# Kernel optimization log

Measured on AMD Instinct MI355X. Metric: run time of the kernel, lower is better.

## Reference

```python
import jax, jax.numpy as jnp
import numpy as np

N, C, E, H = 100000, 128, 640000, 128


def setup_inputs() -> dict:
    key = jax.random.key(0)
    ks = jax.random.split(key, 8)
    x = jax.random.normal(ks[0], (N, C), dtype=jnp.float32)
    # edges guaranteed to have no self-loops (module removes them then re-adds clean self-loops)
    rol = jax.random.randint(ks[1], (E,), 0, N, dtype=jnp.int32)
    off = jax.random.randint(ks[2], (E,), 1, N, dtype=jnp.int32)
    col = (rol + off) % N
    edge_index = jnp.stack([rol, col])  # [2, E]
    s = 1.0 / np.sqrt(C)
    return {
        "x": x,
        "edge_index": edge_index,
        "W_emb": jax.random.normal(ks[3], (C, C), dtype=jnp.float32) * s,
        "b_emb": jnp.zeros((C,), dtype=jnp.float32),
        "Wa1": jax.random.normal(ks[4], (C, H), dtype=jnp.float32) * s,
        "ba1": jnp.zeros((H,), dtype=jnp.float32),
        "Wa2": jax.random.normal(ks[5], (H, 1), dtype=jnp.float32) * (1.0 / np.sqrt(H)),
        "ba2": jnp.zeros((1,), dtype=jnp.float32),
        "W_upd": jax.random.normal(ks[6], (C, C), dtype=jnp.float32) * s,
        "b_upd": jnp.zeros((C,), dtype=jnp.float32),
    }


def reference(x, edge_index, W_emb, b_emb, Wa1, ba1, Wa2, ba2, W_upd, b_upd):
    n = x.shape[0]
    loops = jnp.arange(n, dtype=edge_index.dtype)
    rol = jnp.concatenate([edge_index[0], loops])  # [E+N]
    col = jnp.concatenate([edge_index[1], loops])

    embedded_x = x @ W_emb + b_emb                     # [N, C]
    diff = x[rol] - x[col]                             # [E+N, C]
    h = jax.nn.leaky_relu(diff @ Wa1 + ba1, 0.01)      # [E+N, H]
    a = h @ Wa2 + ba2                                  # [E+N, 1]

    # segment softmax over incoming edges of each target node (col)
    amax = jax.ops.segment_max(a, col, num_segments=n)     # [N, 1]
    ea = jnp.exp(a - amax[col])
    denom = jax.ops.segment_sum(ea, col, num_segments=n)   # [N, 1]
    w = ea / (denom[col] + 1e-16)                           # [E+N, 1]

    msg = jax.ops.segment_sum(embedded_x[rol] * w, col, num_segments=n)  # [N, C]
    return msg @ W_upd + b_upd
```

## Files before the change

### kernel.cpp

```cpp
#include <hip/hip_runtime.h>
#include <hip/hip_bf16.h>

#define LRELU(t) ((t) > 0.0f ? (t) : 0.01f * (t))

__device__ __forceinline__ unsigned short f2bf(float f) {
  unsigned u = __float_as_uint(f);
  u += 0x7fff + ((u >> 16) & 1);
  return (unsigned short)(u >> 16);
}
__device__ __forceinline__ float bflo(unsigned u) { return __uint_as_float(u << 16); }
__device__ __forceinline__ float bfhi(unsigned u) { return __uint_as_float(u & 0xffff0000u); }

template <bool BF16OUT>
__global__ __launch_bounds__(256) void gemm128_kernel(
    const float* __restrict__ A, int lda, const float* __restrict__ B,
    const float* __restrict__ bias, void* __restrict__ Cout, int ldo, int M) {
  __shared__ float Ws[64 * 128];
  __shared__ float Xs[64 * 64];
  const int t = threadIdx.x;
  const int row0 = blockIdx.x * 64;
  const int c0 = (t & 31) * 4;
  const int r0 = (t >> 5) * 8;
  float acc[8][4];
#pragma unroll
  for (int i = 0; i < 8; ++i)
#pragma unroll
    for (int j = 0; j < 4; ++j) acc[i][j] = 0.f;

  for (int kc = 0; kc < 2; ++kc) {
    const int k0 = kc * 64;
#pragma unroll
    for (int i = 0; i < 8; ++i) {
      int f = t + i * 256;
      float4 w4 = *reinterpret_cast<const float4*>(B + (size_t)k0 * 128 + f * 4);
      *reinterpret_cast<float4*>(&Ws[f * 4]) = w4;
    }
#pragma unroll
    for (int i = 0; i < 4; ++i) {
      int f = t + i * 256;
      int r = f >> 4, kq = f & 15;
      float4 x4 = make_float4(0.f, 0.f, 0.f, 0.f);
      int row = row0 + r;
      if (row < M) x4 = *reinterpret_cast<const float4*>(A + (size_t)row * lda + k0 + kq * 4);
      *reinterpret_cast<float4*>(&Xs[r * 64 + kq * 4]) = x4;
    }
    __syncthreads();
#pragma unroll 8
    for (int kk = 0; kk < 64; ++kk) {
      float4 b4 = *reinterpret_cast<const float4*>(&Ws[kk * 128 + c0]);
#pragma unroll
      for (int i = 0; i < 8; ++i) {
        float av = Xs[(r0 + i) * 64 + kk];
        acc[i][0] += av * b4.x;
        acc[i][1] += av * b4.y;
        acc[i][2] += av * b4.z;
        acc[i][3] += av * b4.w;
      }
    }
    __syncthreads();
  }
  float4 bs = make_float4(0.f, 0.f, 0.f, 0.f);
  if (bias) bs = *reinterpret_cast<const float4*>(bias + c0);
#pragma unroll
  for (int i = 0; i < 8; ++i) {
    int row = row0 + r0 + i;
    if (row < M) {
      float vx = acc[i][0] + bs.x, vy = acc[i][1] + bs.y;
      float vz = acc[i][2] + bs.z, vw = acc[i][3] + bs.w;
      if (BF16OUT) {
        ushort4 o;
        o.x = f2bf(vx); o.y = f2bf(vy); o.z = f2bf(vz); o.w = f2bf(vw);
        *reinterpret_cast<ushort4*>((unsigned short*)Cout + (size_t)row * ldo + c0) = o;
      } else {
        float4 o = make_float4(vx, vy, vz, vw);
        *reinterpret_cast<float4*>((float*)Cout + (size_t)row * ldo + c0) = o;
      }
    }
  }
}

__global__ void zero_kernel(int* __restrict__ p, int n) {
  int i = blockIdx.x * blockDim.x + threadIdx.x;
  if (i < n) p[i] = 0;
}

__global__ void count_kernel(const int* __restrict__ col, int* __restrict__ counts, int E) {
  int e = blockIdx.x * blockDim.x + threadIdx.x;
  if (e < E) atomicAdd(&counts[col[e]], 1);
}

__global__ __launch_bounds__(1024) void scan1_kernel(const int* __restrict__ counts,
                                                     int* __restrict__ offsets,
                                                     int* __restrict__ bsum, int N, int N1) {
  __shared__ int sh[1024];
  int tid = threadIdx.x;
  int i = blockIdx.x * 1024 + tid;
  int v = (i < N) ? counts[i] : 0;
  sh[tid] = v;
  __syncthreads();
  for (int off = 1; off < 1024; off <<= 1) {
    int tv = (tid >= off) ? sh[tid - off] : 0;
    __syncthreads();
    sh[tid] += tv;
    __syncthreads();
  }
  if (i < N1) offsets[i] = sh[tid] - v;
  if (tid == 1023) bsum[blockIdx.x] = sh[1023];
}

__global__ __launch_bounds__(128) void scan2_kernel(int* __restrict__ bsum, int NB) {
  __shared__ int sh[128];
  int tid = threadIdx.x;
  int v = (tid < NB) ? bsum[tid] : 0;
  sh[tid] = v;
  __syncthreads();
  for (int off = 1; off < 128; off <<= 1) {
    int tv = (tid >= off) ? sh[tid - off] : 0;
    __syncthreads();
    sh[tid] += tv;
    __syncthreads();
  }
  if (tid < NB) bsum[tid] = sh[tid] - v;
}

__global__ __launch_bounds__(1024) void scan3_kernel(int* __restrict__ offsets,
                                                     const int* __restrict__ bsum,
                                                     int* __restrict__ cursor, int N, int N1) {
  int i = blockIdx.x * 1024 + threadIdx.x;
  if (i < N1) {
    int o = offsets[i] + bsum[blockIdx.x];
    offsets[i] = o;
    if (i < N) cursor[i] = o;
  }
}

__global__ __launch_bounds__(64) void prep_kernel(const float* __restrict__ ba1,
                                                  const float* __restrict__ Wa2,
                                                  const float* __restrict__ ba2,
                                                  float* __restrict__ a_self) {
  int l = threadIdx.x;
  float t1 = ba1[l], t2 = ba1[l + 64];
  float v = LRELU(t1) * Wa2[l] + LRELU(t2) * Wa2[l + 64];
#pragma unroll
  for (int off = 32; off > 0; off >>= 1) v += __shfl_xor(v, off);
  if (l == 0) *a_self = v + ba2[0];
}

__global__ void scatter_kernel(const int* __restrict__ rol, const int* __restrict__ col,
                               int* __restrict__ cursor, int* __restrict__ csr_rol, int E) {
  int e = blockIdx.x * blockDim.x + threadIdx.x;
  if (e < E) {
    int pos = atomicAdd(&cursor[col[e]], 1);
    csr_rol[pos] = rol[e];
  }
}

__global__ __launch_bounds__(256) void fused_kernel(
    const int* __restrict__ offsets, const int* __restrict__ csr_rol,
    const unsigned* __restrict__ embP, const float2* __restrict__ ba1_2,
    const float2* __restrict__ Wa2_2, const float* __restrict__ ba2,
    const float* __restrict__ a_self_p, float* __restrict__ msg, int N, int nwt) {
  const int lane = threadIdx.x & 63;
  const int wid = blockIdx.x * (blockDim.x >> 6) + (threadIdx.x >> 6);
  const float2 b2 = ba1_2[lane];
  const float2 w2 = Wa2_2[lane];
  const float ba2v = *ba2;
  const float aself = *a_self_p;

#define LOGIT(pp) (LRELU(bflo(pp) - pcx + b2.x) * w2.x + LRELU(bfhi(pp) - pcy + b2.y) * w2.y)
#define ONLINE(aval, ue)                      \
  {                                           \
    float nm = fmaxf(m, (aval));              \
    float cc = __expf(m - nm);                \
    float w = __expf((aval)-nm);              \
    s = s * cc + w;                           \
    ax = ax * cc + w * bflo(ue);              \
    ay = ay * cc + w * bfhi(ue);              \
    m = nm;                                   \
  }

  for (int n = wid; n < N; n += nwt) {
    int j0 = offsets[n], j1 = offsets[n + 1];
    unsigned ue_own = embP[(size_t)n * 128 + lane];
    unsigned up_own = embP[(size_t)n * 128 + 64 + lane];
    float pcx = bflo(up_own), pcy = bfhi(up_own);
    float m = aself, s = 1.0f;
    float ax = bflo(ue_own), ay = bfhi(ue_own);
    int j = j0;
    for (; j + 4 <= j1; j += 4) {
      int r0 = csr_rol[j], r1 = csr_rol[j + 1], r2 = csr_rol[j + 2], r3 = csr_rol[j + 3];
      unsigned pe0 = embP[(size_t)r0 * 128 + lane];
      unsigned pp0 = embP[(size_t)r0 * 128 + 64 + lane];
      unsigned pe1 = embP[(size_t)r1 * 128 + lane];
      unsigned pp1 = embP[(size_t)r1 * 128 + 64 + lane];
      unsigned pe2 = embP[(size_t)r2 * 128 + lane];
      unsigned pp2 = embP[(size_t)r2 * 128 + 64 + lane];
      unsigned pe3 = embP[(size_t)r3 * 128 + lane];
      unsigned pp3 = embP[(size_t)r3 * 128 + 64 + lane];
      float v0 = LOGIT(pp0), v1 = LOGIT(pp1), v2 = LOGIT(pp2), v3 = LOGIT(pp3);
#pragma unroll
      for (int off = 32; off > 0; off >>= 1) {
        v0 += __shfl_xor(v0, off);
        v1 += __shfl_xor(v1, off);
        v2 += __shfl_xor(v2, off);
        v3 += __shfl_xor(v3, off);
      }
      ONLINE(v0 + ba2v, pe0);
      ONLINE(v1 + ba2v, pe1);
      ONLINE(v2 + ba2v, pe2);
      ONLINE(v3 + ba2v, pe3);
    }
    for (; j < j1; ++j) {
      int r = csr_rol[j];
      unsigned pe = embP[(size_t)r * 128 + lane];
      unsigned pp = embP[(size_t)r * 128 + 64 + lane];
      float v = LOGIT(pp);
#pragma unroll
      for (int off = 32; off > 0; off >>= 1) v += __shfl_xor(v, off);
      ONLINE(v + ba2v, pe);
    }
    float inv = 1.0f / (s + 1e-16f);
    *reinterpret_cast<float2*>(msg + (size_t)n * 128 + lane * 2) =
        make_float2(ax * inv, ay * inv);
  }
#undef LOGIT
#undef ONLINE
}

extern "C" void kernel_launch(void* const* d_in, const int* in_sizes, int n_in,
                              void* d_out, int out_size, void* d_ws, size_t ws_size,
                              hipStream_t stream) {
  const float* x     = (const float*)d_in[0];
  const int*   ei    = (const int*)d_in[1];
  const float* W_emb = (const float*)d_in[2];
  const float* b_emb = (const float*)d_in[3];
  const float* Wa1   = (const float*)d_in[4];
  const float* ba1   = (const float*)d_in[5];
  const float* Wa2   = (const float*)d_in[6];
  const float* ba2   = (const float*)d_in[7];
  const float* W_upd = (const float*)d_in[8];
  const float* b_upd = (const float*)d_in[9];
  float* out = (float*)d_out;

  const int N = in_sizes[0] / 128;
  const int E = in_sizes[1] / 2;
  const int* rol = ei;
  const int* col = ei + E;

  char* base = (char*)d_ws;
  size_t off = 0;
  auto carve = [&](size_t bytes) {
    void* p = base + off;
    off = (off + bytes + 255) & ~(size_t)255;
    return p;
  };
  unsigned* embP   = (unsigned*)carve((size_t)N * 128 * 4);
  float*    msg    = (float*)carve((size_t)N * 128 * 4);
  int*      csr_rol= (int*)carve((size_t)E * 4);
  float*    a_self = (float*)carve(16);
  int*      counts = (int*)carve((size_t)N * 4);
  int*      offsets= (int*)carve((size_t)(N + 1) * 4);
  int*      cursor = (int*)carve((size_t)N * 4);
  int*      bsum   = (int*)carve(128 * 4);
  (void)ws_size;

  const int N1 = N + 1;
  const int NB = (N1 + 1023) / 1024;
  const int mtiles = (N + 63) / 64;
  const int SBLK = 2048;
  const int NWT = SBLK * 4;

  zero_kernel<<<(N + 255) / 256, 256, 0, stream>>>(counts, N);

  gemm128_kernel<true><<<mtiles, 256, 0, stream>>>(x, 128, W_emb, b_emb, embP, 256, N);
  gemm128_kernel<true><<<mtiles, 256, 0, stream>>>(x, 128, Wa1, nullptr,
                                                   (unsigned short*)embP + 128, 256, N);

  count_kernel<<<(E + 255) / 256, 256, 0, stream>>>(col, counts, E);
  scan1_kernel<<<NB, 1024, 0, stream>>>(counts, offsets, bsum, N, N1);
  scan2_kernel<<<1, 128, 0, stream>>>(bsum, NB);
  scan3_kernel<<<NB, 1024, 0, stream>>>(offsets, bsum, cursor, N, N1);
  prep_kernel<<<1, 64, 0, stream>>>(ba1, Wa2, ba2, a_self);
  scatter_kernel<<<(E + 255) / 256, 256, 0, stream>>>(rol, col, cursor, csr_rol, E);

  fused_kernel<<<SBLK, 256, 0, stream>>>(offsets, csr_rol, embP, (const float2*)ba1,
                                         (const float2*)Wa2, ba2, a_self, msg, N, NWT);

  gemm128_kernel<false><<<mtiles, 256, 0, stream>>>(msg, 128, W_upd, b_upd, out, 128, N);
}
```

Before: 406.3 us.

## Replace scalar FP32 GEMMs with bf16 MFMA kernels and store msg as bf16

Replaces the shared-memory FP32 FMA GEMMs with MFMA 16x16x32 bf16 kernels. Weights are pre-transposed to bf16 by a small kernel, and the two input projections are merged into one 256-column GEMM. The fused aggregation kernel now writes msg as packed bf16, which halves that buffer's traffic and lets the output GEMM read bf16 directly. This lowers precision of the x and msg operands. The epilogue uses scalar, poorly coalesced stores.

```diff
diff --git a/kernel.cpp b/kernel.cpp
--- a/kernel.cpp
+++ b/kernel.cpp
@@ -2,6 +2,9 @@
 #include <hip/hip_bf16.h>
 
 #define LRELU(t) ((t) > 0.0f ? (t) : 0.01f * (t))
+
+typedef __attribute__((ext_vector_type(8))) short bf16x8;
+typedef __attribute__((ext_vector_type(4))) float f32x4;
 
 __device__ __forceinline__ unsigned short f2bf(float f) {
   unsigned u = __float_as_uint(f);
@@ -11,69 +14,129 @@
 __device__ __forceinline__ float bflo(unsigned u) { return __uint_as_float(u << 16); }
 __device__ __forceinline__ float bfhi(unsigned u) { return __uint_as_float(u & 0xffff0000u); }
 
-template <bool BF16OUT>
-__global__ __launch_bounds__(256) void gemm128_kernel(
-    const float* __restrict__ A, int lda, const float* __restrict__ B,
-    const float* __restrict__ bias, void* __restrict__ Cout, int ldo, int M) {
-  __shared__ float Ws[64 * 128];
-  __shared__ float Xs[64 * 64];
-  const int t = threadIdx.x;
+__global__ __launch_bounds__(256) void wtrans_kernel(
+    const float* __restrict__ W_emb, const float* __restrict__ Wa1,
+    const float* __restrict__ W_upd, unsigned short* __restrict__ WtA,
+    unsigned short* __restrict__ WtU) {
+  int i = blockIdx.x * 256 + threadIdx.x;
+  if (i < 32768) {
+    int n = i >> 7, k = i & 127;
+    float v = (n < 128) ? W_emb[k * 128 + n] : Wa1[k * 128 + (n - 128)];
+    WtA[i] = f2bf(v);
+  } else if (i < 49152) {
+    int j = i - 32768;
+    int n = j >> 7, k = j & 127;
+    WtU[j] = f2bf(W_upd[k * 128 + n]);
+  }
+}
+
+__global__ __launch_bounds__(256) void gemm_embP_kernel(
+    const float* __restrict__ A, const unsigned short* __restrict__ Wt,
+    const float* __restrict__ b_emb, unsigned short* __restrict__ C, int M) {
+  const int lane = threadIdx.x & 63;
+  const int w = threadIdx.x >> 6;
   const int row0 = blockIdx.x * 64;
-  const int c0 = (t & 31) * 4;
-  const int r0 = (t >> 5) * 8;
-  float acc[8][4];
-#pragma unroll
-  for (int i = 0; i < 8; ++i)
-#pragma unroll
-    for (int j = 0; j < 4; ++j) acc[i][j] = 0.f;
-
-  for (int kc = 0; kc < 2; ++kc) {
-    const int k0 = kc * 64;
-#pragma unroll
-    for (int i = 0; i < 8; ++i) {
-      int f = t + i * 256;
-      float4 w4 = *reinterpret_cast<const float4*>(B + (size_t)k0 * 128 + f * 4);
-      *reinterpret_cast<float4*>(&Ws[f * 4]) = w4;
-    }
-#pragma unroll
-    for (int i = 0; i < 4; ++i) {
-      int f = t + i * 256;
-      int r = f >> 4, kq = f & 15;
-      float4 x4 = make_float4(0.f, 0.f, 0.f, 0.f);
-      int row = row0 + r;
-      if (row < M) x4 = *reinterpret_cast<const float4*>(A + (size_t)row * lda + k0 + kq * 4);
-      *reinterpret_cast<float4*>(&Xs[r * 64 + kq * 4]) = x4;
-    }
-    __syncthreads();
-#pragma unroll 8
-    for (int kk = 0; kk < 64; ++kk) {
-      float4 b4 = *reinterpret_cast<const float4*>(&Ws[kk * 128 + c0]);
-#pragma unroll
-      for (int i = 0; i < 8; ++i) {
-        float av = Xs[(r0 + i) * 64 + kk];
-        acc[i][0] += av * b4.x;
-        acc[i][1] += av * b4.y;
-        acc[i][2] += av * b4.z;
-        acc[i][3] += av * b4.w;
+  const int ncol0 = w * 64;
+  const int lr = lane & 15;
+  const int lg = lane >> 4;
+  f32x4 acc[4][4];
+#pragma unroll
+  for (int mf = 0; mf < 4; ++mf)
+#pragma unroll
+    for (int nf = 0; nf < 4; ++nf) acc[mf][nf] = (f32x4){0.f, 0.f, 0.f, 0.f};
+
+#pragma unroll
+  for (int ks = 0; ks < 4; ++ks) {
+    const int k0 = ks * 32 + lg * 8;
+    bf16x8 bfr[4];
+#pragma unroll
+    for (int nf = 0; nf < 4; ++nf)
+      bfr[nf] = *reinterpret_cast<const bf16x8*>(Wt + (size_t)(ncol0 + nf * 16 + lr) * 128 + k0);
+    bf16x8 afr[4];
+#pragma unroll
+    for (int mf = 0; mf < 4; ++mf) {
+      int row = row0 + mf * 16 + lr;
+      if (row >= M) row = M - 1;
+      const float* ap = A + (size_t)row * 128 + k0;
+      float4 a0 = *reinterpret_cast<const float4*>(ap);
+      float4 a1 = *reinterpret_cast<const float4*>(ap + 4);
+      bf16x8 t;
+      t[0] = (short)f2bf(a0.x); t[1] = (short)f2bf(a0.y);
+      t[2] = (short)f2bf(a0.z); t[3] = (short)f2bf(a0.w);
+      t[4] = (short)f2bf(a1.x); t[5] = (short)f2bf(a1.y);
+      t[6] = (short)f2bf(a1.z); t[7] = (short)f2bf(a1.w);
+      afr[mf] = t;
+    }
+#pragma unroll
+    for (int mf = 0; mf < 4; ++mf)
+#pragma unroll
+      for (int nf = 0; nf < 4; ++nf)
+        acc[mf][nf] =
+            __builtin_amdgcn_mfma_f32_16x16x32_bf16(afr[mf], bfr[nf], acc[mf][nf], 0, 0, 0);
+  }
+#pragma unroll
+  for (int nf = 0; nf < 4; ++nf) {
+    int col = ncol0 + nf * 16 + lr;
+    float bv = (col < 128) ? b_emb[col] : 0.0f;
+#pragma unroll
+    for (int mf = 0; mf < 4; ++mf) {
+      int rowb = row0 + mf * 16 + lg * 4;
+#pragma unroll
+      for (int r = 0; r < 4; ++r) {
+        int row = rowb + r;
+        if (row < M) C[(size_t)row * 256 + col] = f2bf(acc[mf][nf][r] + bv);
       }
     }
-    __syncthreads();
-  }
-  float4 bs = make_float4(0.f, 0.f, 0.f, 0.f);
-  if (bias) bs = *reinterpret_cast<const float4*>(bias + c0);
-#pragma unroll
-  for (int i = 0; i < 8; ++i) {
-    int row = row0 + r0 + i;
-    if (row < M) {
-      float vx = acc[i][0] + bs.x, vy = acc[i][1] + bs.y;
-      float vz = acc[i][2] + bs.z, vw = acc[i][3] + bs.w;
-      if (BF16OUT) {
-        ushort4 o;
-        o.x = f2bf(vx); o.y = f2bf(vy); o.z = f2bf(vz); o.w = f2bf(vw);
-        *reinterpret_cast<ushort4*>((unsigned short*)Cout + (size_t)row * ldo + c0) = o;
-      } else {
-        float4 o = make_float4(vx, vy, vz, vw);
-        *reinterpret_cast<float4*>((float*)Cout + (size_t)row * ldo + c0) = o;
+  }
+}
+
+__global__ __launch_bounds__(256) void gemm_out_kernel(
+    const unsigned short* __restrict__ Ab, const unsigned short* __restrict__ Wt,
+    const float* __restrict__ b_upd, float* __restrict__ Cout, int M) {
+  const int lane = threadIdx.x & 63;
+  const int w = threadIdx.x >> 6;
+  const int row0 = blockIdx.x * 128 + (w >> 1) * 64;
+  const int ncol0 = (w & 1) * 64;
+  const int lr = lane & 15;
+  const int lg = lane >> 4;
+  f32x4 acc[4][4];
+#pragma unroll
+  for (int mf = 0; mf < 4; ++mf)
+#pragma unroll
+    for (int nf = 0; nf < 4; ++nf) acc[mf][nf] = (f32x4){0.f, 0.f, 0.f, 0.f};
+
+#pragma unroll
+  for (int ks = 0; ks < 4; ++ks) {
+    const int k0 = ks * 32 + lg * 8;
+    bf16x8 bfr[4];
+#pragma unroll
+    for (int nf = 0; nf < 4; ++nf)
+      bfr[nf] = *reinterpret_cast<const bf16x8*>(Wt + (size_t)(ncol0 + nf * 16 + lr) * 128 + k0);
+    bf16x8 afr[4];
+#pragma unroll
+    for (int mf = 0; mf < 4; ++mf) {
+      int row = row0 + mf * 16 + lr;
+      if (row >= M) row = M - 1;
+      afr[mf] = *reinterpret_cast<const bf16x8*>(Ab + (size_t)row * 128 + k0);
+    }
+#pragma unroll
+    for (int mf = 0; mf < 4; ++mf)
+#pragma unroll
+      for (int nf = 0; nf < 4; ++nf)
+        acc[mf][nf] =
+            __builtin_amdgcn_mfma_f32_16x16x32_bf16(afr[mf], bfr[nf], acc[mf][nf], 0, 0, 0);
+  }
+#pragma unroll
+  for (int nf = 0; nf < 4; ++nf) {
+    int col = ncol0 + nf * 16 + lr;
+    float bv = b_upd[col];
+#pragma unroll
+    for (int mf = 0; mf < 4; ++mf) {
+      int rowb = row0 + mf * 16 + lg * 4;
+#pragma unroll
+      for (int r = 0; r < 4; ++r) {
+        int row = rowb + r;
+        if (row < M) Cout[(size_t)row * 128 + col] = acc[mf][nf][r] + bv;
       }
     }
   }
@@ -159,7 +222,7 @@
     const int* __restrict__ offsets, const int* __restrict__ csr_rol,
     const unsigned* __restrict__ embP, const float2* __restrict__ ba1_2,
     const float2* __restrict__ Wa2_2, const float* __restrict__ ba2,
-    const float* __restrict__ a_self_p, float* __restrict__ msg, int N, int nwt) {
+    const float* __restrict__ a_self_p, unsigned* __restrict__ msgb, int N, int nwt) {
   const int lane = threadIdx.x & 63;
   const int wid = blockIdx.x * (blockDim.x >> 6) + (threadIdx.x >> 6);
   const float2 b2 = ba1_2[lane];
@@ -220,8 +283,8 @@
       ONLINE(v + ba2v, pe);
     }
     float inv = 1.0f / (s + 1e-16f);
-    *reinterpret_cast<float2*>(msg + (size_t)n * 128 + lane * 2) =
-        make_float2(ax * inv, ay * inv);
+    msgb[(size_t)n * 64 + lane] =
+        (unsigned)f2bf(ax * inv) | ((unsigned)f2bf(ay * inv) << 16);
   }
 #undef LOGIT
 #undef ONLINE
@@ -255,7 +318,9 @@
     return p;
   };
   unsigned* embP   = (unsigned*)carve((size_t)N * 128 * 4);
-  float*    msg    = (float*)carve((size_t)N * 128 * 4);
+  unsigned* msgb   = (unsigned*)carve((size_t)N * 64 * 4);
+  unsigned short* WtA = (unsigned short*)carve(256 * 128 * 2);
+  unsigned short* WtU = (unsigned short*)carve(128 * 128 * 2);
   int*      csr_rol= (int*)carve((size_t)E * 4);
   float*    a_self = (float*)carve(16);
   int*      counts = (int*)carve((size_t)N * 4);
@@ -266,15 +331,13 @@
 
   const int N1 = N + 1;
   const int NB = (N1 + 1023) / 1024;
-  const int mtiles = (N + 63) / 64;
   const int SBLK = 2048;
   const int NWT = SBLK * 4;
 
   zero_kernel<<<(N + 255) / 256, 256, 0, stream>>>(counts, N);
-
-  gemm128_kernel<true><<<mtiles, 256, 0, stream>>>(x, 128, W_emb, b_emb, embP, 256, N);
-  gemm128_kernel<true><<<mtiles, 256, 0, stream>>>(x, 128, Wa1, nullptr,
-                                                   (unsigned short*)embP + 128, 256, N);
+  wtrans_kernel<<<192, 256, 0, stream>>>(W_emb, Wa1, W_upd, WtA, WtU);
+
+  gemm_embP_kernel<<<(N + 63) / 64, 256, 0, stream>>>(x, WtA, b_emb, (unsigned short*)embP, N);
 
   count_kernel<<<(E + 255) / 256, 256, 0, stream>>>(col, counts, E);
   scan1_kernel<<<NB, 1024, 0, stream>>>(counts, offsets, bsum, N, N1);
@@ -284,7 +347,8 @@
   scatter_kernel<<<(E + 255) / 256, 256, 0, stream>>>(rol, col, cursor, csr_rol, E);
 
   fused_kernel<<<SBLK, 256, 0, stream>>>(offsets, csr_rol, embP, (const float2*)ba1,
-                                         (const float2*)Wa2, ba2, a_self, msg, N, NWT);
-
-  gemm128_kernel<false><<<mtiles, 256, 0, stream>>>(msg, 128, W_upd, b_upd, out, 128, N);
-}
+                                         (const float2*)Wa2, ba2, a_self, msgb, N, NWT);
+
+  gemm_out_kernel<<<(N + 127) / 128, 256, 0, stream>>>((const unsigned short*)msgb, WtU, b_upd,
+                                                       out, N);
+}
```

New measurement: 346.4 us. 14.7% less time.
